# Kernel optimization log

Hardware: AMD Instinct MI355X
Metric: run time of the kernel (lower is better)

The kernel has to match this reference:

```python
import jax, jax.numpy as jnp
import numpy as np

N_NODES = 100000
N_EDGES = 3200000
D = 128
K = 10
NITER = 10


def kmeans(x, K=K, Niter=NITER):
    # c init = first K points, Lloyd iterations (matches the LazyTensor KMeans math)
    N, Dm = x.shape
    c = x[:K, :]
    cl = jnp.zeros((N,), dtype=jnp.int32)
    for _ in range(Niter):
        # argmin_j ||x_i - c_j||^2 == argmin_j (-2 x_i.c_j + ||c_j||^2)
        d = -2.0 * (x @ c.T) + jnp.sum(c * c, axis=-1)  # [N, K]
        cl = jnp.argmin(d, axis=1)
        counts = jax.ops.segment_sum(jnp.ones((N,), x.dtype), cl, num_segments=K)
        sums = jax.ops.segment_sum(x, cl, num_segments=K)
        c = sums / jnp.maximum(counts, 1.0)[:, None]  # guard empty clusters
    return cl, c


def scatter_softmax(scores, seg_ids, num_segments):
    # numerically-stable softmax over edges grouped by seg_ids (torch_geometric.utils.softmax)
    seg_max = jax.ops.segment_max(scores, seg_ids, num_segments=num_segments)
    shifted = jnp.exp(scores - seg_max[seg_ids])
    seg_sum = jax.ops.segment_sum(shifted, seg_ids, num_segments=num_segments)
    return shifted / (seg_sum[seg_ids] + 1e-16)


def setup_inputs() -> dict:
    key = jax.random.key(0)
    k1, k2, k3, k4, k5 = jax.random.split(key, 5)
    x = jax.random.normal(k1, (N_NODES, D), dtype=jnp.float32)
    edge = jax.random.randint(k2, (2, N_EDGES), 0, N_NODES, dtype=jnp.int64)
    # xavier_normal gain 1.414 on [D, D]: std = gain * sqrt(2 / (fan_in + fan_out))
    std = 1.414 * np.sqrt(2.0 / (D + D))
    WQ = jax.random.normal(k3, (D, D), dtype=jnp.float32) * std
    WV = jax.random.normal(k4, (D, D), dtype=jnp.float32) * std
    WK = jax.random.normal(k5, (D, D), dtype=jnp.float32) * std
    return {"x": x, "edge": edge, "WQ": WQ, "WV": WV, "WK": WK}


def reference(x, edge, WQ, WV, WK):
    attention_norm_idx = 0
    alloc, centroids = kmeans(x)                      # [N], [K, D]
    q = centroids @ WQ                                 # [K, D]
    v = centroids @ WV                                 # [K, D]
    prods = (q @ v.T) / jnp.sqrt(jnp.asarray(WK.shape[1], x.dtype))  # [K, K]
    centroid_attention = jax.nn.softmax(prods, axis=1)
    src_c = alloc[edge[0, :]]                          # [E]
    dst_c = alloc[edge[1, :]]                          # [E]
    edge_attention = centroid_attention[src_c, dst_c]  # [E] gather
    attention = scatter_softmax(edge_attention, edge[attention_norm_idx], N_NODES)
    return attention
```

## Files before the change

kernel.cpp:

```cpp
#include <hip/hip_runtime.h>

#define NN 100000
#define NE 3200000
#define DD 128
#define KC 10
#define NITER 10
#define NBK 1024
#define NPAIR (NN / 2)
#define NB4 (NPAIR / 4)
#define NE4 (NE / 4)

template <int CTRL, int RM>
__device__ __forceinline__ float dppadd(float v) {
  int t = __builtin_amdgcn_update_dpp(0, __builtin_bit_cast(int, v), CTRL, RM,
                                      0xF, true);
  return v + __builtin_bit_cast(float, t);
}

__device__ __forceinline__ float halfsum_tail(float v) {
  v = dppadd<0x111, 0xF>(v);
  v = dppadd<0x112, 0xF>(v);
  v = dppadd<0x114, 0xF>(v);
  v = dppadd<0x118, 0xF>(v);
  v = dppadd<0x142, 0xA>(v);
  return v;
}
__device__ __forceinline__ int bcast31i(int v) {
  return __builtin_amdgcn_ds_swizzle(v, 0x3E0);
}

__global__ __launch_bounds__(256, 2) void k_iter6(
    const float* __restrict__ x, const float* __restrict__ csrc,
    float* __restrict__ partial, float* __restrict__ cntpart,
    unsigned char* __restrict__ cl8, int last) {
  __shared__ float cs[KC][DD];
  __shared__ float wsum[4][KC][DD];
  __shared__ float wcnt[4][KC];
  const int tid = threadIdx.x;
  float* wsf = (float*)wsum;
  for (int i = tid; i < KC * DD; i += 256) ((float*)cs)[i] = csrc[i];
  for (int i = tid; i < 4 * KC * DD; i += 256) wsf[i] = 0.f;
  __syncthreads();
  const int w = tid >> 6, lane = tid & 63, half = lane >> 5, hl = lane & 31;

  float4 cfrag[KC];
  float bias[KC];
#pragma unroll
  for (int j = 0; j < KC; ++j) {
    const float4 c4 = *(const float4*)&cs[j][hl * 4];
    cfrag[j] = c4;
    bias[j] = -0.5f * (c4.x * c4.x + c4.y * c4.y + c4.z * c4.z + c4.w * c4.w);
  }
  float cntacc[KC];
#pragma unroll
  for (int j = 0; j < KC; ++j) cntacc[j] = 0.f;

  float* const wrow = &wsum[w][0][hl * 4];
  const float4* __restrict__ x4 = (const float4*)x;
  const int g = blockIdx.x * 4 + w;

  for (int B = g; B < NB4; B += NBK * 4) {
    const size_t rb = (size_t)(8 * B) * 32;
    float4 v[4];
#pragma unroll
    for (int u = 0; u < 4; ++u) v[u] = x4[rb + (size_t)(2 * u + half) * 32 + hl];

#pragma unroll
    for (int u = 0; u < 4; ++u) {
      const int row = 8 * B + 2 * u + half;
      float d[KC];
#pragma unroll
      for (int j = 0; j < KC; ++j)
        d[j] = bias[j] + v[u].x * cfrag[j].x + v[u].y * cfrag[j].y +
               v[u].z * cfrag[j].z + v[u].w * cfrag[j].w;
#pragma unroll
      for (int j = 0; j < KC; ++j) d[j] = halfsum_tail(d[j]);
      int best = 0;
      float bd = d[0];
#pragma unroll
      for (int j = 1; j < KC; ++j) {
        if (d[j] > bd) { bd = d[j]; best = j; }
      }
      const int bown = bcast31i(best);
      const int bother = __shfl_xor(bown, 32);
#pragma unroll
      for (int j = 0; j < KC; ++j)
        cntacc[j] += (bown == j && hl == 0) ? 1.f : 0.f;
      if (last && hl == 0) cl8[row] = (unsigned char)bown;

      if (bown == bother) {
        float4 vs;
        vs.x = v[u].x + __shfl_xor(v[u].x, 32);
        vs.y = v[u].y + __shfl_xor(v[u].y, 32);
        vs.z = v[u].z + __shfl_xor(v[u].z, 32);
        vs.w = v[u].w + __shfl_xor(v[u].w, 32);
        if (half == 0) {
          float4 t = *(float4*)&wrow[bown * DD];
          t.x += vs.x; t.y += vs.y; t.z += vs.z; t.w += vs.w;
          *(float4*)&wrow[bown * DD] = t;
        }
      } else {
        float4 t = *(float4*)&wrow[bown * DD];
        t.x += v[u].x; t.y += v[u].y; t.z += v[u].z; t.w += v[u].w;
        *(float4*)&wrow[bown * DD] = t;
      }
    }
  }
  __syncthreads();
  for (int i = tid; i < KC * DD; i += 256)
    partial[(size_t)blockIdx.x * (KC * DD) + i] =
        wsf[i] + wsf[KC * DD + i] + wsf[2 * KC * DD + i] + wsf[3 * KC * DD + i];
#pragma unroll
  for (int j = 0; j < KC; ++j) cntacc[j] += __shfl_xor(cntacc[j], 32);
  if (half == 0 && hl == 0) {
#pragma unroll
    for (int j = 0; j < KC; ++j) wcnt[w][j] = cntacc[j];
  }
  __syncthreads();
  if (tid < KC)
    cntpart[blockIdx.x * KC + tid] =
        wcnt[0][tid] + wcnt[1][tid] + wcnt[2][tid] + wcnt[3][tid];
}

__global__ __launch_bounds__(256) void k_update2(
    const float* __restrict__ partial, const float* __restrict__ cntpart,
    float* __restrict__ c) {
  const int j = blockIdx.x >> 4, q = blockIdx.x & 15;
  const int tid = threadIdx.x;
  __shared__ float creds[256];
  __shared__ float red2[32][8];
  float cf = 0.f;
#pragma unroll
  for (int m = 0; m < NBK / 256; ++m) cf += cntpart[(tid + 256 * m) * KC + j];
  creds[tid] = cf;
  __syncthreads();
  for (int s = 128; s > 0; s >>= 1) {
    if (tid < s) creds[tid] += creds[tid + s];
    __syncthreads();
  }
  const float denom = fmaxf(creds[0], 1.f);
  const int cc = tid & 7, r = tid >> 3;
  const int col = j * DD + q * 8 + cc;
  float s0 = 0.f;
#pragma unroll 8
  for (int m = 0; m < NBK / 32; ++m)
    s0 += partial[(size_t)(r + 32 * m) * (KC * DD) + col];
  red2[r][cc] = s0;
  __syncthreads();
  if (tid < 8) {
    float t = 0.f;
#pragma unroll
    for (int rr = 0; rr < 32; ++rr) t += red2[rr][tid];
    c[j * DD + q * 8 + tid] = t / denom;
  }
}

__global__ __launch_bounds__(DD) void k_qv(const float* __restrict__ c,
                                           const float* __restrict__ WQ,
                                           const float* __restrict__ WV,
                                           float* __restrict__ qv) {
  const int b = blockIdx.x;
  const int mat = b / KC, i = b % KC;
  const float* __restrict__ W = mat ? WV : WQ;
  __shared__ float cr[DD];
  const int k = threadIdx.x;
  cr[k] = c[i * DD + k];
  __syncthreads();
  float a = 0.f;
#pragma unroll 8
  for (int m = 0; m < DD; ++m) a += cr[m] * W[m * DD + k];
  qv[(size_t)mat * KC * DD + i * DD + k] = a;
}

__global__ __launch_bounds__(DD) void k_att(const float* __restrict__ qv,
                                            float* __restrict__ CA) {
  __shared__ float q[KC][DD + 2], v[KC][DD + 2], pr[KC][KC];
  const int tid = threadIdx.x;
  for (int i = 0; i < KC; ++i) {
    q[i][tid] = qv[i * DD + tid];
    v[i][tid] = qv[KC * DD + i * DD + tid];
  }
  __syncthreads();
  if (tid < KC * KC) {
    const int i = tid / KC, l = tid % KC;
    float acc = 0.f;
#pragma unroll 8
    for (int m = 0; m < DD; ++m) acc += q[i][m] * v[l][m];
    pr[i][l] = acc / sqrtf((float)DD);
  }
  __syncthreads();
  if (tid < KC) {
    float mx = pr[tid][0];
    for (int l = 1; l < KC; ++l) mx = fmaxf(mx, pr[tid][l]);
    float e[KC];
    float s = 0.f;
    for (int l = 0; l < KC; ++l) {
      e[l] = expf(pr[tid][l] - mx);
      s += e[l];
    }
    for (int l = 0; l < KC; ++l) CA[tid * KC + l] = e[l] / s;
  }
}

__global__ __launch_bounds__(256) void k_cnt(const int* __restrict__ e0,
                                             const int* __restrict__ e1,
                                             const unsigned char* __restrict__ cl8,
                                             int* __restrict__ cnt, int base) {
  const int i = base + blockIdx.x * 256 + threadIdx.x;
  if (i >= NE4) return;
  const int4 a = ((const int4*)e0)[i];
  const int4 b = ((const int4*)e1)[i];
  atomicAdd(&cnt[(size_t)a.x * KC + cl8[b.x]], 1);
  atomicAdd(&cnt[(size_t)a.y * KC + cl8[b.y]], 1);
  atomicAdd(&cnt[(size_t)a.z * KC + cl8[b.z]], 1);
  atomicAdd(&cnt[(size_t)a.w * KC + cl8[b.w]], 1);
}

__global__ __launch_bounds__(256) void k_tab2(
    const unsigned char* __restrict__ cl8, const int* __restrict__ cnt,
    const float* __restrict__ CA, float* __restrict__ den) {
  __shared__ float cas[KC * KC];
  __shared__ float rm[KC];
  if (threadIdx.x < KC * KC) cas[threadIdx.x] = CA[threadIdx.x];
  __syncthreads();
  if (threadIdx.x < KC) {
    float m = cas[threadIdx.x * KC];
    for (int l = 1; l < KC; ++l) m = fmaxf(m, cas[threadIdx.x * KC + l]);
    rm[threadIdx.x] = m;
  }
  __syncthreads();
  const int n = blockIdx.x * 256 + threadIdx.x;
  if (n >= NN) return;
  const int s = cl8[n];
  const float m = rm[s];
  float dsum = 0.f;
#pragma unroll
  for (int j = 0; j < KC; ++j) {
    const int cj = cnt[(size_t)n * KC + j];
    dsum += (float)cj * expf(cas[s * KC + j] - m);
  }
  den[n] = dsum;
}

__global__ __launch_bounds__(256) void k_gather2(
    const int* __restrict__ e0, const int* __restrict__ e1,
    const unsigned char* __restrict__ cl8, const float* __restrict__ CA,
    const float* __restrict__ den, float* __restrict__ out) {
  __shared__ float cas[KC * KC];
  __shared__ float rm[KC];
  if (threadIdx.x < KC * KC) cas[threadIdx.x] = CA[threadIdx.x];
  __syncthreads();
  if (threadIdx.x < KC) {
    float m = cas[threadIdx.x * KC];
    for (int l = 1; l < KC; ++l) m = fmaxf(m, cas[threadIdx.x * KC + l]);
    rm[threadIdx.x] = m;
  }
  __syncthreads();
  const int i = blockIdx.x * 256 + threadIdx.x;
  const int4 a = ((const int4*)e0)[i];
  const int4 b = ((const int4*)e1)[i];
  float4 r;
  {
    const int s = cl8[a.x];
    r.x = expf(cas[s * KC + cl8[b.x]] - rm[s]) / (den[a.x] + 1e-16f);
  }
  {
    const int s = cl8[a.y];
    r.y = expf(cas[s * KC + cl8[b.y]] - rm[s]) / (den[a.y] + 1e-16f);
  }
  {
    const int s = cl8[a.z];
    r.z = expf(cas[s * KC + cl8[b.z]] - rm[s]) / (den[a.z] + 1e-16f);
  }
  {
    const int s = cl8[a.w];
    r.w = expf(cas[s * KC + cl8[b.w]] - rm[s]) / (den[a.w] + 1e-16f);
  }
  ((float4*)out)[i] = r;
}

extern "C" void kernel_launch(void* const* d_in, const int* in_sizes, int n_in,
                              void* d_out, int out_size, void* d_ws,
                              size_t ws_size, hipStream_t stream) {
  const float* x = (const float*)d_in[0];
  const int* edge = (const int*)d_in[1];
  const float* WQ = (const float*)d_in[2];
  const float* WV = (const float*)d_in[3];
  float* out = (float*)d_out;
  const int* e0 = edge;
  const int* e1 = edge + NE;

  float* ws = (float*)d_ws;
  float* c = ws;
  float* CA = ws + 1280;
  float* qv = ws + 1392;
  float* den = qv + 2 * KC * DD;
  float* partial = den + NN;
  float* cntpart = partial + (size_t)NBK * KC * DD;
  int* cnt = (int*)(cntpart + NBK * KC);
  unsigned char* cl8 = (unsigned char*)(cnt + (size_t)NN * KC);

  hipMemsetAsync(cnt, 0, (size_t)NN * KC * sizeof(int), stream);

  for (int it = 0; it < NITER; ++it) {
    const float* csrc = (it == 0) ? x : c;
    k_iter6<<<NBK, 256, 0, stream>>>(x, csrc, partial, cntpart, cl8,
                                     it == NITER - 1);
    k_update2<<<KC * 16, 256, 0, stream>>>(partial, cntpart, c);
  }
  k_qv<<<2 * KC, DD, 0, stream>>>(c, WQ, WV, qv);
  k_att<<<1, DD, 0, stream>>>(qv, CA);
  const int TOT_BLKS = (NE4 + 255) / 256;
  const int QB = (TOT_BLKS + 3) / 4;
  for (int q = 0; q < 4; ++q) {
    const int nb = (q < 3) ? QB : (TOT_BLKS - 3 * QB);
    k_cnt<<<nb, 256, 0, stream>>>(e0, e1, cl8, cnt, q * QB * 256);
  }
  k_tab2<<<(NN + 255) / 256, 256, 0, stream>>>(cl8, cnt, CA, den);
  k_gather2<<<NE4 / 256, 256, 0, stream>>>(e0, e1, cl8, CA, den, out);
}
```

Before: 502.6 us.

## Accumulate softmax denominators directly with float atomics, dropping count table pass

Rather than counting edges per (source node, destination cluster) in an N x K integer table and then converting the counts into denominators in a separate per-node kernel, each edge now atomically adds its exponentiated weight straight into a per-node float denominator. Each block precomputes the exponentiated, row-max-shifted attention table in shared memory. This removes the large count table, its memset, and the k_tab2 kernel. The cost is float atomics instead of integer ones, plus an extra cl8 lookup for the source node on every edge, and float atomic accumulation order is nondeterministic.

```diff
diff --git a/kernel.cpp b/kernel.cpp
--- a/kernel.cpp
+++ b/kernel.cpp
@@ -202,44 +202,32 @@
   }
 }
 
-__global__ __launch_bounds__(256) void k_cnt(const int* __restrict__ e0,
+__global__ __launch_bounds__(256) void k_den(const int* __restrict__ e0,
                                              const int* __restrict__ e1,
                                              const unsigned char* __restrict__ cl8,
-                                             int* __restrict__ cnt, int base) {
+                                             const float* __restrict__ CA,
+                                             float* __restrict__ den, int base) {
+  __shared__ float wt[KC * KC];
+  __shared__ float rm[KC];
+  if (threadIdx.x < KC * KC) wt[threadIdx.x] = CA[threadIdx.x];
+  __syncthreads();
+  if (threadIdx.x < KC) {
+    float m = wt[threadIdx.x * KC];
+    for (int l = 1; l < KC; ++l) m = fmaxf(m, wt[threadIdx.x * KC + l]);
+    rm[threadIdx.x] = m;
+  }
+  __syncthreads();
+  if (threadIdx.x < KC * KC)
+    wt[threadIdx.x] = expf(wt[threadIdx.x] - rm[threadIdx.x / KC]);
+  __syncthreads();
   const int i = base + blockIdx.x * 256 + threadIdx.x;
   if (i >= NE4) return;
   const int4 a = ((const int4*)e0)[i];
   const int4 b = ((const int4*)e1)[i];
-  atomicAdd(&cnt[(size_t)a.x * KC + cl8[b.x]], 1);
-  atomicAdd(&cnt[(size_t)a.y * KC + cl8[b.y]], 1);
-  atomicAdd(&cnt[(size_t)a.z * KC + cl8[b.z]], 1);
-  atomicAdd(&cnt[(size_t)a.w * KC + cl8[b.w]], 1);
-}
-
-__global__ __launch_bounds__(256) void k_tab2(
-    const unsigned char* __restrict__ cl8, const int* __restrict__ cnt,
-    const float* __restrict__ CA, float* __restrict__ den) {
-  __shared__ float cas[KC * KC];
-  __shared__ float rm[KC];
-  if (threadIdx.x < KC * KC) cas[threadIdx.x] = CA[threadIdx.x];
-  __syncthreads();
-  if (threadIdx.x < KC) {
-    float m = cas[threadIdx.x * KC];
-    for (int l = 1; l < KC; ++l) m = fmaxf(m, cas[threadIdx.x * KC + l]);
-    rm[threadIdx.x] = m;
-  }
-  __syncthreads();
-  const int n = blockIdx.x * 256 + threadIdx.x;
-  if (n >= NN) return;
-  const int s = cl8[n];
-  const float m = rm[s];
-  float dsum = 0.f;
-#pragma unroll
-  for (int j = 0; j < KC; ++j) {
-    const int cj = cnt[(size_t)n * KC + j];
-    dsum += (float)cj * expf(cas[s * KC + j] - m);
-  }
-  den[n] = dsum;
+  atomicAdd(&den[a.x], wt[cl8[a.x] * KC + cl8[b.x]]);
+  atomicAdd(&den[a.y], wt[cl8[a.y] * KC + cl8[b.y]]);
+  atomicAdd(&den[a.z], wt[cl8[a.z] * KC + cl8[b.z]]);
+  atomicAdd(&den[a.w], wt[cl8[a.w] * KC + cl8[b.w]]);
 }
 
 __global__ __launch_bounds__(256) void k_gather2(
@@ -297,10 +285,9 @@
   float* den = qv + 2 * KC * DD;
   float* partial = den + NN;
   float* cntpart = partial + (size_t)NBK * KC * DD;
-  int* cnt = (int*)(cntpart + NBK * KC);
-  unsigned char* cl8 = (unsigned char*)(cnt + (size_t)NN * KC);
-
-  hipMemsetAsync(cnt, 0, (size_t)NN * KC * sizeof(int), stream);
+  unsigned char* cl8 = (unsigned char*)(cntpart + NBK * KC);
+
+  hipMemsetAsync(den, 0, NN * sizeof(float), stream);
 
   for (int it = 0; it < NITER; ++it) {
     const float* csrc = (it == 0) ? x : c;
@@ -314,8 +301,7 @@
   const int QB = (TOT_BLKS + 3) / 4;
   for (int q = 0; q < 4; ++q) {
     const int nb = (q < 3) ? QB : (TOT_BLKS - 3 * QB);
-    k_cnt<<<nb, 256, 0, stream>>>(e0, e1, cl8, cnt, q * QB * 256);
-  }
-  k_tab2<<<(NN + 255) / 256, 256, 0, stream>>>(cl8, cnt, CA, den);
+    k_den<<<nb, 256, 0, stream>>>(e0, e1, cl8, CA, den, q * QB * 256);
+  }
   k_gather2<<<NE4 / 256, 256, 0, stream>>>(e0, e1, cl8, CA, den, out);
 }
```

Result: slower. 550.6 us (+9.6%).

## Double-buffer x loads in kmeans iteration, pack cluster counts, split count launches

Applied to the files above, without the earlier changes.

Restructures the k-means assignment loop to prefetch the next row block into a second register buffer while the current one is processed, so global load latency overlaps with the distance computation. It replaces ten float per-cluster counters with two packed 6-bit-field integers, cutting register pressure and per-row ALU work. It also splits the edge-count kernel into eight launches instead of four. The extra buffer raises register use, and the packed counters rely on each thread counting at most 63 rows per cluster.

```diff
diff --git a/kernel.cpp b/kernel.cpp
--- a/kernel.cpp
+++ b/kernel.cpp
@@ -51,20 +51,16 @@
     cfrag[j] = c4;
     bias[j] = -0.5f * (c4.x * c4.x + c4.y * c4.y + c4.z * c4.z + c4.w * c4.w);
   }
-  float cntacc[KC];
-#pragma unroll
-  for (int j = 0; j < KC; ++j) cntacc[j] = 0.f;
+  unsigned int cntlo = 0, cnthi = 0;
 
   float* const wrow = &wsum[w][0][hl * 4];
   const float4* __restrict__ x4 = (const float4*)x;
   const int g = blockIdx.x * 4 + w;
-
-  for (int B = g; B < NB4; B += NBK * 4) {
-    const size_t rb = (size_t)(8 * B) * 32;
-    float4 v[4];
-#pragma unroll
-    for (int u = 0; u < 4; ++u) v[u] = x4[rb + (size_t)(2 * u + half) * 32 + hl];
-
+  const int stride = NBK * 4;
+
+  float4 vA[4], vB[4];
+
+  auto compute = [&](const float4* v, int B) {
 #pragma unroll
     for (int u = 0; u < 4; ++u) {
       const int row = 8 * B + 2 * u + half;
@@ -83,9 +79,9 @@
       }
       const int bown = bcast31i(best);
       const int bother = __shfl_xor(bown, 32);
-#pragma unroll
-      for (int j = 0; j < KC; ++j)
-        cntacc[j] += (bown == j && hl == 0) ? 1.f : 0.f;
+      const unsigned sh = 6u * (unsigned)bown;
+      cntlo += (bown < 5) ? (1u << sh) : 0u;
+      cnthi += (bown >= 5) ? (1u << (sh - 30u)) : 0u;
       if (last && hl == 0) cl8[row] = (unsigned char)bown;
 
       if (bown == bother) {
@@ -105,16 +101,39 @@
         *(float4*)&wrow[bown * DD] = t;
       }
     }
+  };
+  auto loadb = [&](float4* v, int B) {
+    const size_t rb = (size_t)(8 * B) * 32;
+#pragma unroll
+    for (int u = 0; u < 4; ++u) v[u] = x4[rb + (size_t)(2 * u + half) * 32 + hl];
+  };
+
+  int B = g;
+  if (B < NB4) {
+    loadb(vA, B);
+    for (;;) {
+      if (B + stride < NB4) loadb(vB, B + stride);
+      compute(vA, B);
+      B += stride;
+      if (B >= NB4) break;
+      if (B + stride < NB4) loadb(vA, B + stride);
+      compute(vB, B);
+      B += stride;
+      if (B >= NB4) break;
+    }
   }
   __syncthreads();
   for (int i = tid; i < KC * DD; i += 256)
     partial[(size_t)blockIdx.x * (KC * DD) + i] =
         wsf[i] + wsf[KC * DD + i] + wsf[2 * KC * DD + i] + wsf[3 * KC * DD + i];
-#pragma unroll
-  for (int j = 0; j < KC; ++j) cntacc[j] += __shfl_xor(cntacc[j], 32);
-  if (half == 0 && hl == 0) {
-#pragma unroll
-    for (int j = 0; j < KC; ++j) wcnt[w][j] = cntacc[j];
+  cntlo += __shfl_xor(cntlo, 32);
+  cnthi += __shfl_xor(cnthi, 32);
+  if (lane == 0) {
+#pragma unroll
+    for (int j = 0; j < 5; ++j) {
+      wcnt[w][j] = (float)((cntlo >> (6 * j)) & 63u);
+      wcnt[w][j + 5] = (float)((cnthi >> (6 * j)) & 63u);
+    }
   }
   __syncthreads();
   if (tid < KC)
@@ -311,10 +330,10 @@
   k_qv<<<2 * KC, DD, 0, stream>>>(c, WQ, WV, qv);
   k_att<<<1, DD, 0, stream>>>(qv, CA);
   const int TOT_BLKS = (NE4 + 255) / 256;
-  const int QB = (TOT_BLKS + 3) / 4;
-  for (int q = 0; q < 4; ++q) {
-    const int nb = (q < 3) ? QB : (TOT_BLKS - 3 * QB);
-    k_cnt<<<nb, 256, 0, stream>>>(e0, e1, cl8, cnt, q * QB * 256);
+  const int QB8 = (TOT_BLKS + 7) / 8;
+  for (int q = 0; q < 8; ++q) {
+    const int nb = (q < 7) ? QB8 : (TOT_BLKS - 7 * QB8);
+    k_cnt<<<nb, 256, 0, stream>>>(e0, e1, cl8, cnt, q * QB8 * 256);
   }
   k_tab2<<<(NN + 255) / 256, 256, 0, stream>>>(cl8, cnt, CA, den);
   k_gather2<<<NE4 / 256, 256, 0, stream>>>(e0, e1, cl8, CA, den, out);
```

After: 502.1 us. No clear change (-0.1%).
